# Optimization experiments

Measured on AMD Instinct MI355X. Metric: run time of the kernel, lower is better.

The kernel has to match this reference:

```python
import jax, jax.numpy as jnp
import numpy as np

N_GRAPHS = 128


def fake_quant4(W):
    # per-tensor symmetric 4-bit weight fake-quant (brevitas-style)
    s = jnp.max(jnp.abs(W)) / 7.0
    q = jnp.clip(jnp.round(W / s), -8.0, 7.0) * s
    # STE: identity gradient through rounding
    return W + jax.lax.stop_gradient(q - W)


def gin_layer(h, src, dst, wa, ba, wb, bb, n_nodes):
    # GIN aggregation: (1+eps)*x + sum_neighbors, eps=0
    agg = jax.ops.segment_sum(h[src], dst, num_segments=n_nodes)  # [N, D]
    h = h + agg
    # int4 weight-only quantized 2-layer MLP
    h = jax.nn.relu(h @ fake_quant4(wa).T + ba)
    return h @ fake_quant4(wb).T + bb


def setup_inputs() -> dict:
    key = jax.random.key(0)
    ks = jax.random.split(key, 16)
    N, E, D = 50000, 800000, 128
    inp = {
        "x": jax.random.normal(ks[0], (N, D), jnp.float32),
        "edge_index": jax.random.randint(ks[1], (2, E), 0, N),
        "batch": jnp.sort(jax.random.randint(ks[2], (N,), 0, N_GRAPHS)),
    }
    for l in range(3):
        inp[f"w{l}a"] = jax.random.normal(ks[3 + 4 * l], (D, D), jnp.float32) * 0.05
        inp[f"b{l}a"] = jnp.zeros((D,), jnp.float32)
        inp[f"w{l}b"] = jax.random.normal(ks[4 + 4 * l], (D, D), jnp.float32) * 0.05
        inp[f"b{l}b"] = jnp.zeros((D,), jnp.float32)
    return inp


def reference(x, edge_index, batch,
              w0a, b0a, w0b, b0b,
              w1a, b1a, w1b, b1b,
              w2a, b2a, w2b, b2b):
    n_nodes = x.shape[0]
    src, dst = edge_index[0], edge_index[1]
    params = [(w0a, b0a, w0b, b0b), (w1a, b1a, w1b, b1b), (w2a, b2a, w2b, b2b)]
    h = x
    for i, (wa, ba, wb, bb) in enumerate(params):
        h = gin_layer(h, src, dst, wa, ba, wb, bb, n_nodes)
        if i < len(params) - 1:
            h = jax.nn.relu(h)  # dropout with p=0 is a no-op
    # global mean pooling over graphs (JK='last')
    sums = jax.ops.segment_sum(h, batch, num_segments=N_GRAPHS)  # [G, D]
    counts = jax.ops.segment_sum(jnp.ones((n_nodes,), h.dtype), batch, num_segments=N_GRAPHS)
    return sums / jnp.maximum(counts, 1.0)[:, None]
```

## Files before the change

kernel.cpp:

```cpp
#include <hip/hip_runtime.h>
#include <math.h>

#define D 128
#define NG 128
#define SLOTS 64

typedef __attribute__((ext_vector_type(8))) unsigned short u16x8;
typedef __attribute__((ext_vector_type(8))) short bf16x8;
typedef __attribute__((ext_vector_type(4))) float f32x4;

__device__ __forceinline__ float bf2f(unsigned short u) {
  return __uint_as_float(((unsigned int)u) << 16);
}
__device__ __forceinline__ unsigned short f2bf(float f) {
  unsigned int u = __float_as_uint(f);
  u += 0x7FFFu + ((u >> 16) & 1u);
  return (unsigned short)(u >> 16);
}

__global__ __launch_bounds__(256) void prep_kernel(
    const float* __restrict__ x, unsigned short* __restrict__ o, int n8,
    const float* __restrict__ w0, const float* __restrict__ w1,
    const float* __restrict__ w2, const float* __restrict__ w3,
    const float* __restrict__ w4, const float* __restrict__ w5,
    unsigned short* __restrict__ qout, int* __restrict__ cnt, int N) {
  int i = blockIdx.x * 256 + threadIdx.x;
  if (i < N) cnt[i] = 0;
  if (i < n8) {
    const float4* xp = reinterpret_cast<const float4*>(x) + (size_t)i * 2;
    float4 a = xp[0], b = xp[1];
    u16x8 v;
    v[0] = f2bf(a.x); v[1] = f2bf(a.y); v[2] = f2bf(a.z); v[3] = f2bf(a.w);
    v[4] = f2bf(b.x); v[5] = f2bf(b.y); v[6] = f2bf(b.z); v[7] = f2bf(b.w);
    *(reinterpret_cast<u16x8*>(o) + i) = v;
  }
  if (blockIdx.x < 6) {
    const float* w;
    switch (blockIdx.x) {
      case 0: w = w0; break;
      case 1: w = w1; break;
      case 2: w = w2; break;
      case 3: w = w3; break;
      case 4: w = w4; break;
      default: w = w5; break;
    }
    unsigned short* q = qout + (size_t)blockIdx.x * (D * D);
    __shared__ float red[256];
    float m = 0.f;
    for (int k = threadIdx.x; k < D * D; k += 256) m = fmaxf(m, fabsf(w[k]));
    red[threadIdx.x] = m;
    __syncthreads();
    for (int s = 128; s > 0; s >>= 1) {
      if (threadIdx.x < s) red[threadIdx.x] = fmaxf(red[threadIdx.x], red[threadIdx.x + s]);
      __syncthreads();
    }
    float s = red[0] / 7.0f;
    for (int k = threadIdx.x; k < D * D; k += 256) {
      float r = rintf(w[k] / s);
      r = fminf(fmaxf(r, -8.f), 7.f);
      q[k] = f2bf((s > 0.f) ? r * s : 0.f);
    }
  }
}

__global__ __launch_bounds__(256) void build_kernel(const int* __restrict__ dst,
                                                    const int* __restrict__ src,
                                                    int* __restrict__ cnt, int* __restrict__ esrc,
                                                    int E, int per_team) {
  int team = blockIdx.x & 7;
  int tb = blockIdx.x >> 3;
  int nb = gridDim.x >> 3;
  int lo = team * per_team;
  int hi = lo + per_team;
  for (int e = tb * 256 + threadIdx.x; e < E; e += nb * 256) {
    int d = dst[e];
    if (d >= lo && d < hi) {
      int slot = atomicAdd(&cnt[d], 1);
      if (slot < SLOTS) esrc[(size_t)d * SLOTS + slot] = src[e];
    }
  }
}

__global__ __launch_bounds__(256) void aggregate_kernel(
    const unsigned short* __restrict__ h, const int* __restrict__ cnt,
    const int* __restrict__ esrc, unsigned short* __restrict__ out, int n) {
  int node = blockIdx.x * 16 + threadIdx.y;
  if (node >= n) return;
  int x = threadIdx.x;
  const u16x8* hp = reinterpret_cast<const u16x8*>(h);
  u16x8 v = hp[(size_t)node * 16 + x];
  float acc[8];
#pragma unroll
  for (int i = 0; i < 8; i++) acc[i] = bf2f(v[i]);
  int c = cnt[node];
  if (c > SLOTS) c = SLOTS;
  const int* base = esrc + (size_t)node * SLOTS;
  int e = 0;
  for (; e + 4 <= c; e += 4) {
    int s0 = base[e], s1 = base[e + 1], s2 = base[e + 2], s3 = base[e + 3];
    u16x8 a0 = hp[(size_t)s0 * 16 + x];
    u16x8 a1 = hp[(size_t)s1 * 16 + x];
    u16x8 a2 = hp[(size_t)s2 * 16 + x];
    u16x8 a3 = hp[(size_t)s3 * 16 + x];
#pragma unroll
    for (int i = 0; i < 8; i++) acc[i] += bf2f(a0[i]) + bf2f(a1[i]);
#pragma unroll
    for (int i = 0; i < 8; i++) acc[i] += bf2f(a2[i]) + bf2f(a3[i]);
  }
  for (; e < c; e++) {
    u16x8 a0 = hp[(size_t)base[e] * 16 + x];
#pragma unroll
    for (int i = 0; i < 8; i++) acc[i] += bf2f(a0[i]);
  }
  u16x8 r;
#pragma unroll
  for (int i = 0; i < 8; i++) r[i] = f2bf(acc[i]);
  reinterpret_cast<u16x8*>(out)[(size_t)node * 16 + x] = r;
}

__global__ __launch_bounds__(256, 3) void mlp_kernel(
    unsigned short* __restrict__ hio, const unsigned short* __restrict__ W1,
    const float* __restrict__ b1, const unsigned short* __restrict__ W2,
    const float* __restrict__ b2, int N, int relu_out) {
  __shared__ unsigned short Wt[128 * D];
  __shared__ unsigned short hs[4][16 * D];
  const int tid = threadIdx.x;
  const int lane = tid & 63;
  const int w = tid >> 6;
  const int c = lane & 15;
  const int q = lane >> 4;

  const int node = blockIdx.x * 64 + w * 16 + c;

  bf16x8 afrag[4];
  if (node < N) {
    const bf16x8* hp = reinterpret_cast<const bf16x8*>(hio);
    size_t rb = (size_t)node * 16;
#pragma unroll
    for (int ks = 0; ks < 4; ks++) afrag[ks] = hp[rb + ks * 4 + q];
  } else {
#pragma unroll
    for (int ks = 0; ks < 4; ks++)
#pragma unroll
      for (int i = 0; i < 8; i++) afrag[ks][i] = 0;
  }

#pragma unroll
  for (int i = 0; i < 8; i++) {
    int gid = tid + 256 * i;
    int row = gid >> 4;
    int g = gid & 15;
    *reinterpret_cast<u16x8*>(&Wt[row * D + (g ^ (row & 15)) * 8]) =
        *reinterpret_cast<const u16x8*>(W1 + (size_t)row * D + g * 8);
  }
  __syncthreads();

  f32x4 acc1[8] = {};
#pragma unroll
  for (int ks = 0; ks < 4; ks++) {
    int g = ks * 4 + q;
#pragma unroll
    for (int j = 0; j < 8; j++) {
      bf16x8 b = *reinterpret_cast<const bf16x8*>(&Wt[(j * 16 + c) * D + ((g ^ c) * 8)]);
      acc1[j] = __builtin_amdgcn_mfma_f32_16x16x32_bf16(afrag[ks], b, acc1[j], 0, 0, 0);
    }
  }

  unsigned short* tile = &hs[w][0];
#pragma unroll
  for (int j = 0; j < 8; j++) {
    int col = j * 16 + c;
    float bb = b1[col];
    int gcol = col >> 3;
    int el = col & 7;
#pragma unroll
    for (int r = 0; r < 4; r++) {
      int row = q * 4 + r;
      float v = fmaxf(acc1[j][r] + bb, 0.f);
      tile[row * D + ((gcol ^ row) * 8) + el] = f2bf(v);
    }
  }
  __syncthreads();

#pragma unroll
  for (int i = 0; i < 8; i++) {
    int gid = tid + 256 * i;
    int row = gid >> 4;
    int g = gid & 15;
    *reinterpret_cast<u16x8*>(&Wt[row * D + (g ^ (row & 15)) * 8]) =
        *reinterpret_cast<const u16x8*>(W2 + (size_t)row * D + g * 8);
  }
  __syncthreads();

  f32x4 acc2[8] = {};
#pragma unroll
  for (int ks = 0; ks < 4; ks++) {
    int g = ks * 4 + q;
    bf16x8 a = *reinterpret_cast<const bf16x8*>(&tile[c * D + ((g ^ c) * 8)]);
#pragma unroll
    for (int j = 0; j < 8; j++) {
      bf16x8 b = *reinterpret_cast<const bf16x8*>(&Wt[(j * 16 + c) * D + ((g ^ c) * 8)]);
      acc2[j] = __builtin_amdgcn_mfma_f32_16x16x32_bf16(a, b, acc2[j], 0, 0, 0);
    }
  }

#pragma unroll
  for (int j = 0; j < 8; j++) {
    int col = j * 16 + c;
    float bb = b2[col];
#pragma unroll
    for (int r = 0; r < 4; r++) {
      int rnode = blockIdx.x * 64 + w * 16 + q * 4 + r;
      if (rnode < N) {
        float v = acc2[j][r] + bb;
        if (relu_out) v = fmaxf(v, 0.f);
        hio[(size_t)rnode * D + col] = f2bf(v);
      }
    }
  }
}

__global__ __launch_bounds__(256) void pool_partial(const unsigned short* __restrict__ h,
                                                    const int* __restrict__ batch, int n,
                                                    float* __restrict__ partials,
                                                    float* __restrict__ counts) {
  int g = blockIdx.x;
  int s = blockIdx.y;
  __shared__ int sbeg, send;
  if (threadIdx.x == 0) {
    int lo = 0, hi = n;
    while (lo < hi) { int mid = (lo + hi) >> 1; if (batch[mid] < g) lo = mid + 1; else hi = mid; }
    sbeg = lo;
    hi = n;
    while (lo < hi) { int mid = (lo + hi) >> 1; if (batch[mid] < g + 1) lo = mid + 1; else hi = mid; }
    send = lo;
    if (s == 0) counts[g] = (float)(send - sbeg);
  }
  __syncthreads();
  int beg = sbeg, end = send;
  int x = threadIdx.x & 15;
  int ty = threadIdx.x >> 4;
  const u16x8* hp = reinterpret_cast<const u16x8*>(h);
  float acc[8] = {};
  for (int i = beg + s * 16 + ty; i < end; i += 128) {
    u16x8 v = hp[(size_t)i * 16 + x];
#pragma unroll
    for (int k = 0; k < 8; k++) acc[k] += bf2f(v[k]);
  }
  __shared__ float red[16][16][8];
#pragma unroll
  for (int k = 0; k < 8; k++) red[ty][x][k] = acc[k];
  __syncthreads();
  for (int st = 8; st > 0; st >>= 1) {
    if (ty < st) {
#pragma unroll
      for (int k = 0; k < 8; k++) red[ty][x][k] += red[ty + st][x][k];
    }
    __syncthreads();
  }
  if (ty == 0) {
#pragma unroll
    for (int k = 0; k < 8; k++)
      partials[((size_t)s * NG + g) * D + x * 8 + k] = red[0][x][k];
  }
}

__global__ __launch_bounds__(256) void pool_final(const float* __restrict__ partials,
                                                  const float* __restrict__ counts,
                                                  float* __restrict__ out) {
  int idx = blockIdx.x * 256 + threadIdx.x;
  if (idx >= NG * D) return;
  int g = idx >> 7;
  int d = idx & 127;
  float sum = 0.f;
#pragma unroll
  for (int s = 0; s < 8; s++) sum += partials[((size_t)s * NG + g) * D + d];
  out[idx] = sum / fmaxf(counts[g], 1.0f);
}

extern "C" void kernel_launch(void* const* d_in, const int* in_sizes, int n_in,
                              void* d_out, int out_size, void* d_ws, size_t ws_size,
                              hipStream_t stream) {
  const float* x = (const float*)d_in[0];
  const int* ei = (const int*)d_in[1];
  const int* batch = (const int*)d_in[2];
  const float* w[6] = {(const float*)d_in[3], (const float*)d_in[5],
                       (const float*)d_in[7], (const float*)d_in[9],
                       (const float*)d_in[11], (const float*)d_in[13]};
  const float* b[6] = {(const float*)d_in[4], (const float*)d_in[6],
                       (const float*)d_in[8], (const float*)d_in[10],
                       (const float*)d_in[12], (const float*)d_in[14]};
  const int N = in_sizes[0] / D;
  const int E = in_sizes[1] / 2;
  const int* src = ei;
  const int* dst = ei + E;

  char* ws = (char*)d_ws;
  size_t off = 0;
  auto carve = [&](size_t bytes) -> char* {
    char* p = ws + off;
    off = (off + bytes + 255) & ~(size_t)255;
    return p;
  };
  unsigned short* hA = (unsigned short*)carve((size_t)N * D * 2);
  unsigned short* hB = (unsigned short*)carve((size_t)N * D * 2);
  unsigned short* qw = (unsigned short*)carve(6 * D * D * 2);
  int* cnt = (int*)carve((size_t)N * 4);
  int* esrc = (int*)carve((size_t)N * SLOTS * 4);
  float* partials = (float*)carve((size_t)8 * NG * D * 4);
  float* counts = (float*)carve((size_t)NG * 4);
  if (off > ws_size) return;

  int n8 = N * D / 8;
  int prepGrid = (n8 + 255) / 256;
  if (prepGrid < 6) prepGrid = 6;
  int nzGrid = (N + 255) / 256;
  if (prepGrid < nzGrid) prepGrid = nzGrid;
  prep_kernel<<<prepGrid, 256, 0, stream>>>(x, hA, n8, w[0], w[1], w[2], w[3], w[4], w[5], qw, cnt, N);

  int bGrid = ((E + 255) / 256 + 7) & ~7;
  int per_team = (N + 7) / 8;
  build_kernel<<<bGrid, 256, 0, stream>>>(dst, src, cnt, esrc, E, per_team);

  dim3 aggBlock(16, 16);
  int aggGrid = (N + 15) / 16;
  int mlpGrid = (N + 63) / 64;
  unsigned short* cur = hA;
  unsigned short* oth = hB;
  for (int l = 0; l < 3; ++l) {
    aggregate_kernel<<<aggGrid, aggBlock, 0, stream>>>(cur, cnt, esrc, oth, N);
    mlp_kernel<<<mlpGrid, 256, 0, stream>>>(oth, qw + (size_t)(2 * l) * D * D, b[2 * l],
                                            qw + (size_t)(2 * l + 1) * D * D, b[2 * l + 1], N,
                                            (l < 2) ? 1 : 0);
    unsigned short* t = cur; cur = oth; oth = t;
  }

  dim3 ppGrid(NG, 8);
  pool_partial<<<ppGrid, 256, 0, stream>>>(cur, batch, N, partials, counts);
  pool_final<<<(NG * D + 255) / 256, 256, 0, stream>>>(partials, counts, (float*)d_out);
}
```

Before: 225.8 us.

## Fuse neighbor aggregation and MLP into one 16-node-per-block layer kernel

```diff
diff --git a/kernel.cpp b/kernel.cpp
--- a/kernel.cpp
+++ b/kernel.cpp
@@ -81,95 +81,83 @@
   }
 }
 
-__global__ __launch_bounds__(256) void aggregate_kernel(
+__global__ __launch_bounds__(256) void layer16_kernel(
     const unsigned short* __restrict__ h, const int* __restrict__ cnt,
-    const int* __restrict__ esrc, unsigned short* __restrict__ out, int n) {
-  int node = blockIdx.x * 16 + threadIdx.y;
-  if (node >= n) return;
-  int x = threadIdx.x;
-  const u16x8* hp = reinterpret_cast<const u16x8*>(h);
-  u16x8 v = hp[(size_t)node * 16 + x];
-  float acc[8];
-#pragma unroll
-  for (int i = 0; i < 8; i++) acc[i] = bf2f(v[i]);
-  int c = cnt[node];
-  if (c > SLOTS) c = SLOTS;
-  const int* base = esrc + (size_t)node * SLOTS;
-  int e = 0;
-  for (; e + 4 <= c; e += 4) {
-    int s0 = base[e], s1 = base[e + 1], s2 = base[e + 2], s3 = base[e + 3];
-    u16x8 a0 = hp[(size_t)s0 * 16 + x];
-    u16x8 a1 = hp[(size_t)s1 * 16 + x];
-    u16x8 a2 = hp[(size_t)s2 * 16 + x];
-    u16x8 a3 = hp[(size_t)s3 * 16 + x];
-#pragma unroll
-    for (int i = 0; i < 8; i++) acc[i] += bf2f(a0[i]) + bf2f(a1[i]);
-#pragma unroll
-    for (int i = 0; i < 8; i++) acc[i] += bf2f(a2[i]) + bf2f(a3[i]);
-  }
-  for (; e < c; e++) {
-    u16x8 a0 = hp[(size_t)base[e] * 16 + x];
-#pragma unroll
-    for (int i = 0; i < 8; i++) acc[i] += bf2f(a0[i]);
-  }
-  u16x8 r;
-#pragma unroll
-  for (int i = 0; i < 8; i++) r[i] = f2bf(acc[i]);
-  reinterpret_cast<u16x8*>(out)[(size_t)node * 16 + x] = r;
-}
-
-__global__ __launch_bounds__(256, 3) void mlp_kernel(
-    unsigned short* __restrict__ hio, const unsigned short* __restrict__ W1,
+    const int* __restrict__ esrc, const unsigned short* __restrict__ W1,
     const float* __restrict__ b1, const unsigned short* __restrict__ W2,
-    const float* __restrict__ b2, int N, int relu_out) {
-  __shared__ unsigned short Wt[128 * D];
-  __shared__ unsigned short hs[4][16 * D];
+    const float* __restrict__ b2, unsigned short* __restrict__ out, int N, int relu_out) {
+  __shared__ unsigned short Atile[16 * D];
+  __shared__ unsigned short Htile[16 * D];
   const int tid = threadIdx.x;
+
+  {
+    int x = tid & 15;
+    int y = tid >> 4;
+    int node = blockIdx.x * 16 + y;
+    const u16x8* hp = reinterpret_cast<const u16x8*>(h);
+    u16x8 r;
+    if (node < N) {
+      u16x8 v = hp[(size_t)node * 16 + x];
+      float acc[8];
+#pragma unroll
+      for (int i = 0; i < 8; i++) acc[i] = bf2f(v[i]);
+      int c = cnt[node];
+      if (c > SLOTS) c = SLOTS;
+      const int* base = esrc + (size_t)node * SLOTS;
+      int e = 0;
+      for (; e + 4 <= c; e += 4) {
+        int s0 = base[e], s1 = base[e + 1], s2 = base[e + 2], s3 = base[e + 3];
+        u16x8 a0 = hp[(size_t)s0 * 16 + x];
+        u16x8 a1 = hp[(size_t)s1 * 16 + x];
+        u16x8 a2 = hp[(size_t)s2 * 16 + x];
+        u16x8 a3 = hp[(size_t)s3 * 16 + x];
+#pragma unroll
+        for (int i = 0; i < 8; i++) acc[i] += bf2f(a0[i]) + bf2f(a1[i]);
+#pragma unroll
+        for (int i = 0; i < 8; i++) acc[i] += bf2f(a2[i]) + bf2f(a3[i]);
+      }
+      for (; e < c; e++) {
+        u16x8 a0 = hp[(size_t)base[e] * 16 + x];
+#pragma unroll
+        for (int i = 0; i < 8; i++) acc[i] += bf2f(a0[i]);
+      }
+#pragma unroll
+      for (int i = 0; i < 8; i++) r[i] = f2bf(acc[i]);
+    } else {
+#pragma unroll
+      for (int i = 0; i < 8; i++) r[i] = 0;
+    }
+    *reinterpret_cast<u16x8*>(&Atile[y * D + ((x ^ y) * 8)]) = r;
+  }
+  __syncthreads();
+
   const int lane = tid & 63;
   const int w = tid >> 6;
   const int c = lane & 15;
   const int q = lane >> 4;
 
-  const int node = blockIdx.x * 64 + w * 16 + c;
-
   bf16x8 afrag[4];
-  if (node < N) {
-    const bf16x8* hp = reinterpret_cast<const bf16x8*>(hio);
-    size_t rb = (size_t)node * 16;
-#pragma unroll
-    for (int ks = 0; ks < 4; ks++) afrag[ks] = hp[rb + ks * 4 + q];
-  } else {
-#pragma unroll
-    for (int ks = 0; ks < 4; ks++)
-#pragma unroll
-      for (int i = 0; i < 8; i++) afrag[ks][i] = 0;
-  }
-
-#pragma unroll
-  for (int i = 0; i < 8; i++) {
-    int gid = tid + 256 * i;
-    int row = gid >> 4;
-    int g = gid & 15;
-    *reinterpret_cast<u16x8*>(&Wt[row * D + (g ^ (row & 15)) * 8]) =
-        *reinterpret_cast<const u16x8*>(W1 + (size_t)row * D + g * 8);
-  }
-  __syncthreads();
-
-  f32x4 acc1[8] = {};
 #pragma unroll
   for (int ks = 0; ks < 4; ks++) {
     int g = ks * 4 + q;
-#pragma unroll
-    for (int j = 0; j < 8; j++) {
-      bf16x8 b = *reinterpret_cast<const bf16x8*>(&Wt[(j * 16 + c) * D + ((g ^ c) * 8)]);
+    afrag[ks] = *reinterpret_cast<const bf16x8*>(&Atile[c * D + ((g ^ c) * 8)]);
+  }
+
+  f32x4 acc1[2] = {};
+#pragma unroll
+  for (int ks = 0; ks < 4; ks++) {
+    int g = ks * 4 + q;
+#pragma unroll
+    for (int j = 0; j < 2; j++) {
+      int jj = w * 2 + j;
+      bf16x8 b = *reinterpret_cast<const bf16x8*>(W1 + (size_t)(jj * 16 + c) * D + g * 8);
       acc1[j] = __builtin_amdgcn_mfma_f32_16x16x32_bf16(afrag[ks], b, acc1[j], 0, 0, 0);
     }
   }
 
-  unsigned short* tile = &hs[w][0];
-#pragma unroll
-  for (int j = 0; j < 8; j++) {
-    int col = j * 16 + c;
+#pragma unroll
+  for (int j = 0; j < 2; j++) {
+    int col = (w * 2 + j) * 16 + c;
     float bb = b1[col];
     int gcol = col >> 3;
     int el = col & 7;
@@ -177,44 +165,40 @@
     for (int r = 0; r < 4; r++) {
       int row = q * 4 + r;
       float v = fmaxf(acc1[j][r] + bb, 0.f);
-      tile[row * D + ((gcol ^ row) * 8) + el] = f2bf(v);
+      Htile[row * D + ((gcol ^ row) * 8) + el] = f2bf(v);
     }
   }
   __syncthreads();
 
-#pragma unroll
-  for (int i = 0; i < 8; i++) {
-    int gid = tid + 256 * i;
-    int row = gid >> 4;
-    int g = gid & 15;
-    *reinterpret_cast<u16x8*>(&Wt[row * D + (g ^ (row & 15)) * 8]) =
-        *reinterpret_cast<const u16x8*>(W2 + (size_t)row * D + g * 8);
-  }
-  __syncthreads();
-
-  f32x4 acc2[8] = {};
+  bf16x8 hfrag[4];
 #pragma unroll
   for (int ks = 0; ks < 4; ks++) {
     int g = ks * 4 + q;
-    bf16x8 a = *reinterpret_cast<const bf16x8*>(&tile[c * D + ((g ^ c) * 8)]);
-#pragma unroll
-    for (int j = 0; j < 8; j++) {
-      bf16x8 b = *reinterpret_cast<const bf16x8*>(&Wt[(j * 16 + c) * D + ((g ^ c) * 8)]);
-      acc2[j] = __builtin_amdgcn_mfma_f32_16x16x32_bf16(a, b, acc2[j], 0, 0, 0);
-    }
-  }
-
-#pragma unroll
-  for (int j = 0; j < 8; j++) {
-    int col = j * 16 + c;
+    hfrag[ks] = *reinterpret_cast<const bf16x8*>(&Htile[c * D + ((g ^ c) * 8)]);
+  }
+  f32x4 acc2[2] = {};
+#pragma unroll
+  for (int ks = 0; ks < 4; ks++) {
+    int g = ks * 4 + q;
+#pragma unroll
+    for (int j = 0; j < 2; j++) {
+      int jj = w * 2 + j;
+      bf16x8 b = *reinterpret_cast<const bf16x8*>(W2 + (size_t)(jj * 16 + c) * D + g * 8);
+      acc2[j] = __builtin_amdgcn_mfma_f32_16x16x32_bf16(hfrag[ks], b, acc2[j], 0, 0, 0);
+    }
+  }
+
+#pragma unroll
+  for (int j = 0; j < 2; j++) {
+    int col = (w * 2 + j) * 16 + c;
     float bb = b2[col];
 #pragma unroll
     for (int r = 0; r < 4; r++) {
-      int rnode = blockIdx.x * 64 + w * 16 + q * 4 + r;
-      if (rnode < N) {
+      int node = blockIdx.x * 16 + q * 4 + r;
+      if (node < N) {
         float v = acc2[j][r] + bb;
         if (relu_out) v = fmaxf(v, 0.f);
-        hio[(size_t)rnode * D + col] = f2bf(v);
+        out[(size_t)node * D + col] = f2bf(v);
       }
     }
   }
@@ -322,16 +306,13 @@
   int per_team = (N + 7) / 8;
   build_kernel<<<bGrid, 256, 0, stream>>>(dst, src, cnt, esrc, E, per_team);
 
-  dim3 aggBlock(16, 16);
-  int aggGrid = (N + 15) / 16;
-  int mlpGrid = (N + 63) / 64;
+  int grid = (N + 15) / 16;
   unsigned short* cur = hA;
   unsigned short* oth = hB;
   for (int l = 0; l < 3; ++l) {
-    aggregate_kernel<<<aggGrid, aggBlock, 0, stream>>>(cur, cnt, esrc, oth, N);
-    mlp_kernel<<<mlpGrid, 256, 0, stream>>>(oth, qw + (size_t)(2 * l) * D * D, b[2 * l],
-                                            qw + (size_t)(2 * l + 1) * D * D, b[2 * l + 1], N,
-                                            (l < 2) ? 1 : 0);
+    layer16_kernel<<<grid, 256, 0, stream>>>(cur, cnt, esrc, qw + (size_t)(2 * l) * D * D, b[2 * l],
+                                             qw + (size_t)(2 * l + 1) * D * D, b[2 * l + 1], oth, N,
+                                             (l < 2) ? 1 : 0);
     unsigned short* t = cur; cur = oth; oth = t;
   }
 
```

New measurement: 248.1 us. 9.9% more time.
